# Optimization experiments

Measured on AMD Instinct MI355X. Metric: run time of the kernel, lower is better.

## Reference

```python
import jax, jax.numpy as jnp
import numpy as np

EPS = 1e-5
SCALE_MIN, SCALE_MAX = 0.6, 1.0


def _layer_norm(x):
    m = jnp.mean(x, axis=-1, keepdims=True)
    v = jnp.mean((x - m) ** 2, axis=-1, keepdims=True)
    return (x - m) / jnp.sqrt(v + EPS)


def _scan_dir(seq, A, Bp, Cp, D, W_in, W_out, snr_scale):
    """seq: [B, L, C] -> [B, L, C]. Diagonal SSM recurrence h = A*h + B*u."""
    Bsz, L, C = seq.shape
    N = A.shape[0]
    seq = _layer_norm(seq)
    u = jnp.einsum('blc,nc->bln', seq, W_in)                 # input_proj, [B,L,N]
    A_base = jnp.tanh(A)[None, :]                            # [1,N]
    s = jnp.clip(snr_scale, 0.0, 1.0)[:, None]               # [B,1]
    scale = SCALE_MIN + (SCALE_MAX - SCALE_MIN) * s
    Ad = jnp.clip(A_base * scale, -0.99, 0.99)               # [B,N]
    Bu = Bp[None, None, :] * u                               # [B,L,N]

    def step(h, bu_t):
        h = Ad * h + bu_t
        return h, h

    h0 = jnp.zeros((Bsz, N), dtype=seq.dtype)
    _, hs = jax.lax.scan(step, h0, jnp.swapaxes(Bu, 0, 1))   # hs: [L,B,N]
    hs = jnp.swapaxes(hs, 0, 1)                              # [B,L,N]
    y_state = Cp[None, None, :] * hs
    y = jnp.einsum('bln,cn->blc', y_state, W_out)            # output_proj
    return y + D[None, None, :] * seq


def _forward(x, snr_scale, A, Bparam, Cparam, D, W_in, W_out):
    Bsz, H, W, C = x.shape
    L = H * W
    if L > 4000:
        x = _layer_norm(x)
    # row scans
    seq_row = x.reshape(Bsz, L, C)
    y_row_f = _scan_dir(seq_row, A, Bparam, Cparam, D, W_in, W_out, snr_scale)
    y_row_b = _scan_dir(seq_row[:, ::-1, :], A, Bparam, Cparam, D, W_in, W_out, snr_scale)
    y_row = 0.5 * (y_row_f + y_row_b[:, ::-1, :])
    y_row = y_row.reshape(Bsz, H, W, C)
    # column scans
    x_col = jnp.transpose(x, (0, 2, 1, 3))                   # [B,W,H,C]
    seq_col = x_col.reshape(Bsz, L, C)
    y_col_f = _scan_dir(seq_col, A, Bparam, Cparam, D, W_in, W_out, snr_scale)
    y_col_b = _scan_dir(seq_col[:, ::-1, :], A, Bparam, Cparam, D, W_in, W_out, snr_scale)
    y_col = 0.5 * (y_col_f + y_col_b[:, ::-1, :])
    y_col = jnp.transpose(y_col.reshape(Bsz, W, H, C), (0, 2, 1, 3))
    return 0.5 * (y_row + y_col)


def setup_inputs() -> dict:
    key = jax.random.key(0)
    k = jax.random.split(key, 4)
    Bsz, H, W, C, N = 8, 64, 64, 256, 64
    x = jax.random.normal(k[0], (Bsz, H, W, C), dtype=jnp.float32)
    snr_scale = jax.random.uniform(k[1], (Bsz,), dtype=jnp.float32)
    A = -0.5 * jnp.ones((N,), dtype=jnp.float32)
    Bparam = 0.5 * jnp.ones((N,), dtype=jnp.float32)
    Cparam = 0.5 * jnp.ones((N,), dtype=jnp.float32)
    D = jnp.zeros((C,), dtype=jnp.float32)
    # nn.Linear default init: U(-1/sqrt(fan_in), 1/sqrt(fan_in))
    W_in = jax.random.uniform(k[2], (N, C), dtype=jnp.float32,
                              minval=-1.0 / np.sqrt(C), maxval=1.0 / np.sqrt(C))
    W_out = jax.random.uniform(k[3], (C, N), dtype=jnp.float32,
                               minval=-1.0 / np.sqrt(N), maxval=1.0 / np.sqrt(N))
    return {"x": x, "snr_scale": snr_scale, "A": A, "Bparam": Bparam,
            "Cparam": Cparam, "D": D, "W_in": W_in, "W_out": W_out}


def reference(x, snr_scale, A, Bparam, Cparam, D, W_in, W_out):
    return _forward(x, snr_scale, A, Bparam, Cparam, D, W_in, W_out)
```

## Files before the change

### kernel.cpp

```cpp
#include <hip/hip_runtime.h>
#include <hip/hip_bf16.h>
#include <math.h>

#define Bsz 8
#define Hh 64
#define Ww 64
#define Cc 256
#define Nn 64
#define Ll 4096
#define EPSf 1e-5f

typedef __bf16 v8bf __attribute__((ext_vector_type(8)));
typedef float  f32x4 __attribute__((ext_vector_type(4)));

__device__ __forceinline__ float ad_val(float a, float snr) {
    float s = fminf(fmaxf(snr, 0.f), 1.f);
    float scale = 0.6f + 0.4f * s;
    float v = tanhf(a) * scale;
    return fminf(fmaxf(v, -0.99f), 0.99f);
}

__global__ __launch_bounds__(256) void k0_weights(
    const float* __restrict__ Win, const float* __restrict__ Wout,
    const float* __restrict__ Bp, const float* __restrict__ Cp,
    __bf16* __restrict__ Wh, __bf16* __restrict__ Wl,
    __bf16* __restrict__ Woh, __bf16* __restrict__ Wol,
    float* __restrict__ WB)
{
    const int t = threadIdx.x;
    const int blk = blockIdx.x;
    if (blk < 4) {
        for (int idx = blk * 512 + t; idx < blk * 512 + 512; idx += 256) {
            int tile = idx >> 6, lane = idx & 63;
            int kt = tile >> 2, nt = tile & 3;
            int q = lane >> 4, n = nt * 16 + (lane & 15);
            #pragma unroll
            for (int j = 0; j < 8; ++j) {
                int k = kt * 32 + q * 8 + j;
                float w = Win[n * Cc + k];
                __bf16 h = (__bf16)w;
                Wh[idx * 8 + j] = h;
                Wl[idx * 8 + j] = (__bf16)(w - (float)h);
            }
        }
    } else if (blk < 8) {
        for (int idx = (blk - 4) * 512 + t; idx < (blk - 4) * 512 + 512; idx += 256) {
            int tile = idx >> 6, lane = idx & 63;
            int kt = tile >> 4, ntg = tile & 15;
            int q = lane >> 4, c = ntg * 16 + (lane & 15);
            #pragma unroll
            for (int j = 0; j < 8; ++j) {
                int k = kt * 32 + q * 8 + j;
                float w = Wout[c * Nn + k] * 0.25f * Cp[k];
                __bf16 h = (__bf16)w;
                Woh[idx * 8 + j] = h;
                Wol[idx * 8 + j] = (__bf16)(w - (float)h);
            }
        }
    } else {
        __shared__ float wtmp[256];
        int n = t >> 2, qd = t & 3;
        float s = 0.f;
        const float* wr = Win + (long)n * Cc + qd * 64;
        for (int i = 0; i < 64; ++i) s += wr[i];
        wtmp[t] = s;
        __syncthreads();
        if (t < 64)
            WB[t] = (wtmp[t*4] + wtmp[t*4+1] + wtmp[t*4+2] + wtmp[t*4+3]) * Bp[t];
    }
}

__global__ __launch_bounds__(256) void k1_ln_gemm(
    const float* __restrict__ x, const __bf16* __restrict__ Wh,
    const __bf16* __restrict__ Wl, const float* __restrict__ Bp,
    const float* __restrict__ WB, float* __restrict__ Bu,
    float* __restrict__ Mst, float* __restrict__ Sst)
{
    __shared__ float mrow[64], srow[64];
    const int t = threadIdx.x;
    const int lane = t & 63;
    const int wv = __builtin_amdgcn_readfirstlane(t >> 6);
    const long pbase = (long)blockIdx.x * 64;
    const float* xt = x + pbase * Cc;

    for (int rr = 0; rr < 16; ++rr) {
        int r = wv * 16 + rr;
        float4 v = ((const float4*)(xt + (long)r * Cc))[lane];
        float s = v.x + v.y + v.z + v.w;
        float q = v.x*v.x + v.y*v.y + v.z*v.z + v.w*v.w;
        #pragma unroll
        for (int off = 32; off > 0; off >>= 1) {
            s += __shfl_down(s, off);
            q += __shfl_down(q, off);
        }
        if (lane == 0) {
            float m = s * (1.f/256.f);
            float var = fmaxf(q * (1.f/256.f) - m*m, 0.f);
            float r1 = rsqrtf(var + EPSf);
            float v2 = var / (var + EPSf);
            float sc = r1 * rsqrtf(v2 + EPSf);
            mrow[r] = m; srow[r] = sc;
            Mst[pbase + r] = m; Sst[pbase + r] = sc;
        }
    }
    __syncthreads();

    const int q = lane >> 4;
    const int mi = lane & 15;
    const float* xa = xt + (long)(wv * 16 + mi) * Cc + q * 8;

    f32x4 acc[4];
    #pragma unroll
    for (int nt = 0; nt < 4; ++nt) acc[nt] = (f32x4){0.f, 0.f, 0.f, 0.f};

    #pragma unroll
    for (int kt = 0; kt < 8; ++kt) {
        float4 a0 = *(const float4*)(xa + kt * 32);
        float4 a1 = *(const float4*)(xa + kt * 32 + 4);
        float av[8] = {a0.x, a0.y, a0.z, a0.w, a1.x, a1.y, a1.z, a1.w};
        v8bf ah, al;
        #pragma unroll
        for (int j = 0; j < 8; ++j) {
            __bf16 h = (__bf16)av[j];
            ah[j] = h;
            al[j] = (__bf16)(av[j] - (float)h);
        }
        #pragma unroll
        for (int nt = 0; nt < 4; ++nt) {
            v8bf bh = *(const v8bf*)(Wh + ((long)(kt * 4 + nt) * 64 + lane) * 8);
            v8bf bl = *(const v8bf*)(Wl + ((long)(kt * 4 + nt) * 64 + lane) * 8);
            acc[nt] = __builtin_amdgcn_mfma_f32_16x16x32_bf16(ah, bh, acc[nt], 0, 0, 0);
            acc[nt] = __builtin_amdgcn_mfma_f32_16x16x32_bf16(al, bh, acc[nt], 0, 0, 0);
            acc[nt] = __builtin_amdgcn_mfma_f32_16x16x32_bf16(ah, bl, acc[nt], 0, 0, 0);
        }
    }

    #pragma unroll
    for (int nt = 0; nt < 4; ++nt) {
        int n = nt * 16 + mi;
        float bpn = Bp[n];
        float wbn = WB[n];
        #pragma unroll
        for (int reg = 0; reg < 4; ++reg) {
            int p = wv * 16 + q * 4 + reg;
            float m = mrow[p], s = srow[p];
            Bu[(pbase + p) * Nn + n] = s * (acc[nt][reg] * bpn - m * wbn);
        }
    }
}

__global__ __launch_bounds__(256) void k2_carry(
    const float* __restrict__ Bu, const float* __restrict__ A,
    const float* __restrict__ snr, float* __restrict__ E)
{
    const int t = threadIdx.x;
    const int lane = t & 63;
    const int task = blockIdx.x * 4 + (t >> 6);
    const int isCol = task >> 9;
    const int b = (task >> 6) & 7;
    const int j = task & 63;
    const float Ad = ad_val(A[lane], snr[b]);
    const float* src = Bu + ((long)b * Ll + (isCol ? j : j * 64)) * Nn + lane;
    const long stride = isCol ? (long)Ww * Nn : Nn;

    float v[64];
    #pragma unroll
    for (int k = 0; k < 64; ++k) v[k] = src[k * stride];

    float s = 0.f;
    #pragma unroll
    for (int k = 0; k < 64; ++k) s = fmaf(Ad, s, v[k]);
    const int dF = isCol ? 2 : 0;
    E[((dF * 8 + b) * 64 + j) * 64 + lane] = s;

    float sb = 0.f;
    #pragma unroll
    for (int k = 63; k >= 0; --k) sb = fmaf(Ad, sb, v[k]);
    E[(((dF + 1) * 8 + b) * 64 + (63 - j)) * 64 + lane] = sb;
}

__global__ __launch_bounds__(64) void k3_prefix(
    const float* __restrict__ E, float* __restrict__ CT,
    const float* __restrict__ A, const float* __restrict__ snr)
{
    const int lane = threadIdx.x;
    const int db = blockIdx.x;
    const int b = db & 7;
    float Ad = ad_val(A[lane], snr[b]);
    float p64 = Ad;
    #pragma unroll
    for (int i = 0; i < 6; ++i) p64 *= p64;
    const float* e = E + (long)db * 4096 + lane;
    float* ct = CT + (long)db * 4096 + lane;
    float v[64];
    #pragma unroll
    for (int k = 0; k < 64; ++k) v[k] = e[k * 64];
    float c = 0.f;
    #pragma unroll
    for (int k = 0; k < 64; ++k) {
        ct[k * 64] = c;
        c = fmaf(p64, c, v[k]);
    }
}

__global__ __launch_bounds__(256) void k4_apply(
    const float* __restrict__ Bu, const float* __restrict__ CT,
    const float* __restrict__ A, const float* __restrict__ snr,
    float* __restrict__ Srow, float* __restrict__ Scol)
{
    const int t = threadIdx.x;
    const int lane = t & 63;
    const int task = blockIdx.x * 4 + (t >> 6);
    const int isCol = task >> 9;
    const int b = (task >> 6) & 7;
    const int j = task & 63;
    const float Ad = ad_val(A[lane], snr[b]);
    const float* src = Bu + ((long)b * Ll + (isCol ? j : j * 64)) * Nn + lane;
    const long stride = isCol ? (long)Ww * Nn : Nn;
    const int dF = isCol ? 2 : 0;
    const float cf = CT[((dF * 8 + b) * 64 + j) * 64 + lane];
    const float cb = CT[(((dF + 1) * 8 + b) * 64 + (63 - j)) * 64 + lane];

    float v[64];
    #pragma unroll
    for (int k = 0; k < 64; ++k) v[k] = src[k * stride];

    float hf[64];
    float h = cf;
    #pragma unroll
    for (int k = 0; k < 64; ++k) { h = fmaf(Ad, h, v[k]); hf[k] = h; }

    float* out0 = (isCol ? Scol : Srow) +
                  ((long)b * Ll + (isCol ? j : j * 64)) * Nn + lane;
    float sb = cb;
    #pragma unroll
    for (int k = 63; k >= 0; --k) {
        sb = fmaf(Ad, sb, v[k]);
        out0[k * stride] = hf[k] + sb;
    }
}

__global__ __launch_bounds__(256) void k5_gemm_out(
    const float* __restrict__ Srow, const float* __restrict__ Scol,
    const float* __restrict__ x, const __bf16* __restrict__ Woh,
    const __bf16* __restrict__ Wol, const float* __restrict__ Dp,
    const float* __restrict__ Mst, const float* __restrict__ Sst,
    float* __restrict__ out)
{
    __shared__ float smem[64 * 260];
    const int t = threadIdx.x;
    const int lane = t & 63;
    const int wv = __builtin_amdgcn_readfirstlane(t >> 6);
    const long pbase = (long)blockIdx.x * 64;
    const int q = lane >> 4;
    const int mi = lane & 15;

    const float4* Sr = (const float4*)(Srow + pbase * Nn);
    const float4* Sc = (const float4*)(Scol + pbase * Nn);
    #pragma unroll
    for (int i = 0; i < 4; ++i) {
        int fi = i * 256 + t;
        float4 a = Sr[fi], c = Sc[fi];
        *(float4*)&smem[(fi >> 4) * 68 + (fi & 15) * 4] =
            make_float4(a.x + c.x, a.y + c.y, a.z + c.z, a.w + c.w);
    }
    __syncthreads();

    f32x4 acc[4][4];
    #pragma unroll
    for (int mt = 0; mt < 4; ++mt)
        #pragma unroll
        for (int nt = 0; nt < 4; ++nt) acc[mt][nt] = (f32x4){0.f, 0.f, 0.f, 0.f};

    #pragma unroll
    for (int kt = 0; kt < 2; ++kt) {
        v8bf bh[4], bl[4];
        #pragma unroll
        for (int nt = 0; nt < 4; ++nt) {
            long wo = ((long)(kt * 16 + wv * 4 + nt) * 64 + lane) * 8;
            bh[nt] = *(const v8bf*)(Woh + wo);
            bl[nt] = *(const v8bf*)(Wol + wo);
        }
        #pragma unroll
        for (int mt = 0; mt < 4; ++mt) {
            const float* ar = &smem[(mt * 16 + mi) * 68 + q * 8 + kt * 32];
            v8bf sh, sl;
            #pragma unroll
            for (int j = 0; j < 8; ++j) {
                float sv = ar[j];
                __bf16 hh = (__bf16)sv;
                sh[j] = hh;
                sl[j] = (__bf16)(sv - (float)hh);
            }
            #pragma unroll
            for (int nt = 0; nt < 4; ++nt) {
                acc[mt][nt] = __builtin_amdgcn_mfma_f32_16x16x32_bf16(sh, bh[nt], acc[mt][nt], 0, 0, 0);
                acc[mt][nt] = __builtin_amdgcn_mfma_f32_16x16x32_bf16(sl, bh[nt], acc[mt][nt], 0, 0, 0);
                acc[mt][nt] = __builtin_amdgcn_mfma_f32_16x16x32_bf16(sh, bl[nt], acc[mt][nt], 0, 0, 0);
            }
        }
    }
    __syncthreads();
    #pragma unroll
    for (int mt = 0; mt < 4; ++mt)
        #pragma unroll
        for (int nt = 0; nt < 4; ++nt) {
            int c = wv * 64 + nt * 16 + mi;
            #pragma unroll
            for (int reg = 0; reg < 4; ++reg)
                smem[(mt * 16 + q * 4 + reg) * 260 + c] = acc[mt][nt][reg];
        }
    __syncthreads();

    const float4* xg = (const float4*)(x + pbase * Cc);
    float4* og = (float4*)(out + pbase * Cc);
    const float4 dv = ((const float4*)Dp)[lane];
    #pragma unroll 4
    for (int i = 0; i < 16; ++i) {
        int fi = i * 256 + t;
        int p = i * 4 + wv;
        float4 v = *(const float4*)&smem[p * 260 + lane * 4];
        float m = Mst[pbase + p], s = Sst[pbase + p];
        float4 xv = xg[fi];
        og[fi] = make_float4(v.x + dv.x * ((xv.x - m) * s),
                             v.y + dv.y * ((xv.y - m) * s),
                             v.z + dv.z * ((xv.z - m) * s),
                             v.w + dv.w * ((xv.w - m) * s));
    }
}

extern "C" void kernel_launch(void* const* d_in, const int* in_sizes, int n_in,
                              void* d_out, int out_size, void* d_ws, size_t ws_size,
                              hipStream_t stream)
{
    const float* x    = (const float*)d_in[0];
    const float* snr  = (const float*)d_in[1];
    const float* A    = (const float*)d_in[2];
    const float* Bp   = (const float*)d_in[3];
    const float* Cp   = (const float*)d_in[4];
    const float* Dp   = (const float*)d_in[5];
    const float* Win  = (const float*)d_in[6];
    const float* Wout = (const float*)d_in[7];
    float* out = (float*)d_out;

    char* ws = (char*)d_ws;
    float*  Bu   = (float*)(ws);
    float*  Srow = (float*)(ws + (size_t)8  * 1024 * 1024);
    float*  Scol = (float*)(ws + (size_t)16 * 1024 * 1024);
    float*  E    = (float*)(ws + (size_t)24 * 1024 * 1024);
    float*  CT   = (float*)(ws + (size_t)24 * 1024 * 1024 + 512*1024);
    float*  Mst  = (float*)(ws + (size_t)25 * 1024 * 1024);
    float*  Sst  = (float*)(ws + (size_t)25 * 1024 * 1024 + 128*1024);
    char*   wbase = ws + (size_t)25 * 1024 * 1024 + 512 * 1024;
    __bf16* Wh   = (__bf16*)(wbase);
    __bf16* Wl   = (__bf16*)(wbase + 32 * 1024);
    __bf16* Woh  = (__bf16*)(wbase + 64 * 1024);
    __bf16* Wol  = (__bf16*)(wbase + 96 * 1024);
    float*  WB   = (float*)(wbase + 128 * 1024);

    hipLaunchKernelGGL(k0_weights,  dim3(9),   dim3(256), 0, stream, Win, Wout, Bp, Cp, Wh, Wl, Woh, Wol, WB);
    hipLaunchKernelGGL(k1_ln_gemm,  dim3(512), dim3(256), 0, stream, x, Wh, Wl, Bp, WB, Bu, Mst, Sst);
    hipLaunchKernelGGL(k2_carry,    dim3(256), dim3(256), 0, stream, Bu, A, snr, E);
    hipLaunchKernelGGL(k3_prefix,   dim3(32),  dim3(64),  0, stream, E, CT, A, snr);
    hipLaunchKernelGGL(k4_apply,    dim3(256), dim3(256), 0, stream, Bu, CT, A, snr, Srow, Scol);
    hipLaunchKernelGGL(k5_gemm_out, dim3(512), dim3(256), 0, stream, Srow, Scol, x, Woh, Wol, Dp, Mst, Sst, out);
}
```

Measured before the change: 138.4 us.

## Split scan chunks across wave pairs, fold prefix kernel into apply, halve epilogue LDS

Each 64-step scan chunk is now split across two waves of 32 steps. In the carry kernel the halves are combined through LDS, and partial sums are stored for later seeding. The separate prefix kernel is removed, and the apply kernel recomputes its carry-in by looping serially over the preceding chunk totals. The output GEMM epilogue stages results through LDS in two 32-row halves, halving shared memory to raise occupancy. In exchange, apply threads do redundant serial prefix work of up to 63 strided loads each, and extra syncs are added.

```diff
diff --git a/kernel.cpp b/kernel.cpp
--- a/kernel.cpp
+++ b/kernel.cpp
@@ -151,90 +151,99 @@
 
 __global__ __launch_bounds__(256) void k2_carry(
     const float* __restrict__ Bu, const float* __restrict__ A,
-    const float* __restrict__ snr, float* __restrict__ E)
-{
+    const float* __restrict__ snr, float* __restrict__ E,
+    float* __restrict__ Pf, float* __restrict__ Pb)
+{
+    __shared__ float exch[2][2][64];
     const int t = threadIdx.x;
     const int lane = t & 63;
-    const int task = blockIdx.x * 4 + (t >> 6);
+    const int wv = t >> 6;
+    const int pairIdx = wv >> 1;
+    const int half = wv & 1;
+    const int task = blockIdx.x * 2 + pairIdx;
     const int isCol = task >> 9;
     const int b = (task >> 6) & 7;
     const int j = task & 63;
     const float Ad = ad_val(A[lane], snr[b]);
-    const float* src = Bu + ((long)b * Ll + (isCol ? j : j * 64)) * Nn + lane;
+    float p32 = Ad;
+    #pragma unroll
+    for (int i = 0; i < 5; ++i) p32 *= p32;
     const long stride = isCol ? (long)Ww * Nn : Nn;
-
-    float v[64];
-    #pragma unroll
-    for (int k = 0; k < 64; ++k) v[k] = src[k * stride];
-
-    float s = 0.f;
-    #pragma unroll
-    for (int k = 0; k < 64; ++k) s = fmaf(Ad, s, v[k]);
-    const int dF = isCol ? 2 : 0;
-    E[((dF * 8 + b) * 64 + j) * 64 + lane] = s;
-
-    float sb = 0.f;
-    #pragma unroll
-    for (int k = 63; k >= 0; --k) sb = fmaf(Ad, sb, v[k]);
-    E[(((dF + 1) * 8 + b) * 64 + (63 - j)) * 64 + lane] = sb;
-}
-
-__global__ __launch_bounds__(64) void k3_prefix(
-    const float* __restrict__ E, float* __restrict__ CT,
-    const float* __restrict__ A, const float* __restrict__ snr)
-{
-    const int lane = threadIdx.x;
-    const int db = blockIdx.x;
-    const int b = db & 7;
-    float Ad = ad_val(A[lane], snr[b]);
-    float p64 = Ad;
-    #pragma unroll
-    for (int i = 0; i < 6; ++i) p64 *= p64;
-    const float* e = E + (long)db * 4096 + lane;
-    float* ct = CT + (long)db * 4096 + lane;
-    float v[64];
-    #pragma unroll
-    for (int k = 0; k < 64; ++k) v[k] = e[k * 64];
-    float c = 0.f;
-    #pragma unroll
-    for (int k = 0; k < 64; ++k) {
-        ct[k * 64] = c;
-        c = fmaf(p64, c, v[k]);
+    const float* src = Bu + ((long)b * Ll + (isCol ? j : j * 64)) * Nn
+                       + (long)half * 32 * stride + lane;
+    float v[32];
+    #pragma unroll
+    for (int k = 0; k < 32; ++k) v[k] = src[k * stride];
+    float pf = 0.f;
+    #pragma unroll
+    for (int k = 0; k < 32; ++k) pf = fmaf(Ad, pf, v[k]);
+    float pb = 0.f;
+    #pragma unroll
+    for (int k = 31; k >= 0; --k) pb = fmaf(Ad, pb, v[k]);
+    if (half) { exch[pairIdx][0][lane] = pf; exch[pairIdx][1][lane] = pb; }
+    __syncthreads();
+    if (!half) {
+        const int dF = isCol ? 2 : 0;
+        float pf_hi = exch[pairIdx][0][lane];
+        float pb_hi = exch[pairIdx][1][lane];
+        E[((dF * 8 + b) * 64 + j) * 64 + lane]              = fmaf(p32, pf, pf_hi);
+        E[(((dF + 1) * 8 + b) * 64 + (63 - j)) * 64 + lane] = fmaf(p32, pb_hi, pb);
+        Pf[task * 64 + lane] = pf;
+        Pb[task * 64 + lane] = pb_hi;
     }
 }
 
 __global__ __launch_bounds__(256) void k4_apply(
-    const float* __restrict__ Bu, const float* __restrict__ CT,
+    const float* __restrict__ Bu, const float* __restrict__ E,
+    const float* __restrict__ Pf, const float* __restrict__ Pb,
     const float* __restrict__ A, const float* __restrict__ snr,
     float* __restrict__ Srow, float* __restrict__ Scol)
 {
     const int t = threadIdx.x;
     const int lane = t & 63;
-    const int task = blockIdx.x * 4 + (t >> 6);
+    const int wv = t >> 6;
+    const int task = blockIdx.x * 2 + (wv >> 1);
+    const int half = wv & 1;
     const int isCol = task >> 9;
     const int b = (task >> 6) & 7;
     const int j = task & 63;
     const float Ad = ad_val(A[lane], snr[b]);
-    const float* src = Bu + ((long)b * Ll + (isCol ? j : j * 64)) * Nn + lane;
+    float p32 = Ad;
+    #pragma unroll
+    for (int i = 0; i < 5; ++i) p32 *= p32;
+    float p64 = p32 * p32;
+    const int dF = isCol ? 2 : 0;
+
+    const float* Ef = E + (long)((dF * 8 + b) * 64) * 64 + lane;
+    const float* Eb = E + (long)(((dF + 1) * 8 + b) * 64) * 64 + lane;
+    float cf = 0.f;
+    #pragma unroll 4
+    for (int i = 0; i < j; ++i) cf = fmaf(p64, cf, Ef[i * 64]);
+    float cb = 0.f;
+    const int jj = 63 - j;
+    #pragma unroll 4
+    for (int i = 0; i < jj; ++i) cb = fmaf(p64, cb, Eb[i * 64]);
+
+    float fseed = half ? fmaf(p32, cf, Pf[task * 64 + lane]) : cf;
+    float bseed = half ? cb : fmaf(p32, cb, Pb[task * 64 + lane]);
+
     const long stride = isCol ? (long)Ww * Nn : Nn;
-    const int dF = isCol ? 2 : 0;
-    const float cf = CT[((dF * 8 + b) * 64 + j) * 64 + lane];
-    const float cb = CT[(((dF + 1) * 8 + b) * 64 + (63 - j)) * 64 + lane];
-
-    float v[64];
-    #pragma unroll
-    for (int k = 0; k < 64; ++k) v[k] = src[k * stride];
-
-    float hf[64];
-    float h = cf;
-    #pragma unroll
-    for (int k = 0; k < 64; ++k) { h = fmaf(Ad, h, v[k]); hf[k] = h; }
-
-    float* out0 = (isCol ? Scol : Srow) +
-                  ((long)b * Ll + (isCol ? j : j * 64)) * Nn + lane;
-    float sb = cb;
-    #pragma unroll
-    for (int k = 63; k >= 0; --k) {
+    const long base = ((long)b * Ll + (isCol ? j : j * 64)) * Nn
+                      + (long)half * 32 * stride + lane;
+    const float* src = Bu + base;
+    float v[32];
+    #pragma unroll
+    for (int k = 0; k < 32; ++k) v[k] = src[k * stride];
+
+    float hf[32];
+    float h = fseed;
+    #pragma unroll
+    for (int k = 0; k < 32; ++k) { h = fmaf(Ad, h, v[k]); hf[k] = h; }
+
+    float* out0 = (isCol ? Scol : Srow) + base;
+    float sb = bseed;
+    #pragma unroll
+    for (int k = 31; k >= 0; --k) {
         sb = fmaf(Ad, sb, v[k]);
         out0[k * stride] = hf[k] + sb;
     }
@@ -247,7 +256,7 @@
     const float* __restrict__ Mst, const float* __restrict__ Sst,
     float* __restrict__ out)
 {
-    __shared__ float smem[64 * 260];
+    __shared__ float smem[32 * 260];
     const int t = threadIdx.x;
     const int lane = t & 63;
     const int wv = __builtin_amdgcn_readfirstlane(t >> 6);
@@ -300,32 +309,39 @@
             }
         }
     }
-    __syncthreads();
-    #pragma unroll
-    for (int mt = 0; mt < 4; ++mt)
-        #pragma unroll
-        for (int nt = 0; nt < 4; ++nt) {
-            int c = wv * 64 + nt * 16 + mi;
-            #pragma unroll
-            for (int reg = 0; reg < 4; ++reg)
-                smem[(mt * 16 + q * 4 + reg) * 260 + c] = acc[mt][nt][reg];
-        }
-    __syncthreads();
 
     const float4* xg = (const float4*)(x + pbase * Cc);
     float4* og = (float4*)(out + pbase * Cc);
     const float4 dv = ((const float4*)Dp)[lane];
-    #pragma unroll 4
-    for (int i = 0; i < 16; ++i) {
-        int fi = i * 256 + t;
-        int p = i * 4 + wv;
-        float4 v = *(const float4*)&smem[p * 260 + lane * 4];
-        float m = Mst[pbase + p], s = Sst[pbase + p];
-        float4 xv = xg[fi];
-        og[fi] = make_float4(v.x + dv.x * ((xv.x - m) * s),
-                             v.y + dv.y * ((xv.y - m) * s),
-                             v.z + dv.z * ((xv.z - m) * s),
-                             v.w + dv.w * ((xv.w - m) * s));
+    #pragma unroll
+    for (int hh = 0; hh < 2; ++hh) {
+        __syncthreads();
+        #pragma unroll
+        for (int mt2 = 0; mt2 < 2; ++mt2) {
+            int mt = hh * 2 + mt2;
+            #pragma unroll
+            for (int nt = 0; nt < 4; ++nt) {
+                int c = wv * 64 + nt * 16 + mi;
+                #pragma unroll
+                for (int reg = 0; reg < 4; ++reg)
+                    smem[(mt2 * 16 + q * 4 + reg) * 260 + c] = acc[mt][nt][reg];
+            }
+        }
+        __syncthreads();
+        #pragma unroll 4
+        for (int i = 0; i < 8; ++i) {
+            int fi = i * 256 + t;
+            int pl = i * 4 + wv;
+            long pg = pbase + hh * 32 + pl;
+            float4 vv = *(const float4*)&smem[pl * 260 + lane * 4];
+            float m = Mst[pg], s = Sst[pg];
+            float4 xv = xg[hh * 2048 + fi];
+            og[hh * 2048 + fi] = make_float4(
+                vv.x + dv.x * ((xv.x - m) * s),
+                vv.y + dv.y * ((xv.y - m) * s),
+                vv.z + dv.z * ((xv.z - m) * s),
+                vv.w + dv.w * ((xv.w - m) * s));
+        }
     }
 }
 
@@ -348,7 +364,8 @@
     float*  Srow = (float*)(ws + (size_t)8  * 1024 * 1024);
     float*  Scol = (float*)(ws + (size_t)16 * 1024 * 1024);
     float*  E    = (float*)(ws + (size_t)24 * 1024 * 1024);
-    float*  CT   = (float*)(ws + (size_t)24 * 1024 * 1024 + 512*1024);
+    float*  Pf   = (float*)(ws + (size_t)24 * 1024 * 1024 + 512*1024);
+    float*  Pb   = (float*)(ws + (size_t)24 * 1024 * 1024 + 768*1024);
     float*  Mst  = (float*)(ws + (size_t)25 * 1024 * 1024);
     float*  Sst  = (float*)(ws + (size_t)25 * 1024 * 1024 + 128*1024);
     char*   wbase = ws + (size_t)25 * 1024 * 1024 + 512 * 1024;
@@ -360,8 +377,7 @@
 
     hipLaunchKernelGGL(k0_weights,  dim3(9),   dim3(256), 0, stream, Win, Wout, Bp, Cp, Wh, Wl, Woh, Wol, WB);
     hipLaunchKernelGGL(k1_ln_gemm,  dim3(512), dim3(256), 0, stream, x, Wh, Wl, Bp, WB, Bu, Mst, Sst);
-    hipLaunchKernelGGL(k2_carry,    dim3(256), dim3(256), 0, stream, Bu, A, snr, E);
-    hipLaunchKernelGGL(k3_prefix,   dim3(32),  dim3(64),  0, stream, E, CT, A, snr);
-    hipLaunchKernelGGL(k4_apply,    dim3(256), dim3(256), 0, stream, Bu, CT, A, snr, Srow, Scol);
+    hipLaunchKernelGGL(k2_carry,    dim3(512), dim3(256), 0, stream, Bu, A, snr, E, Pf, Pb);
+    hipLaunchKernelGGL(k4_apply,    dim3(512), dim3(256), 0, stream, Bu, E, Pf, Pb, A, snr, Srow, Scol);
     hipLaunchKernelGGL(k5_gemm_out, dim3(512), dim3(256), 0, stream, Srow, Scol, x, Woh, Wol, Dp, Mst, Sst, out);
 }
```

New measurement: 156.1 us. +12.8%, slower.

## Fuse row-direction scan carry and apply into the input and output GEMM kernels

Applied to the files above, without the earlier changes.

The row-direction scan work moves out of the standalone carry and apply kernels. k1 now computes each block's row-segment carries from the Bu tile it has just produced in shared memory. k5 recomputes the row-direction scan states locally from Bu and the prefix carries, then adds the column states before the output GEMM. This removes the Srow buffer and its global write and read, and halves the grid of the column-only scan kernels. In exchange, k5 uses more shared memory and more barriers, and its epilogue staging is split into two halves to fit the smaller buffer.

```diff
diff --git a/kernel.cpp b/kernel.cpp
--- a/kernel.cpp
+++ b/kernel.cpp
@@ -73,29 +73,34 @@
 __global__ __launch_bounds__(256) void k1_ln_gemm(
     const float* __restrict__ x, const __bf16* __restrict__ Wh,
     const __bf16* __restrict__ Wl, const float* __restrict__ Bp,
-    const float* __restrict__ WB, float* __restrict__ Bu,
-    float* __restrict__ Mst, float* __restrict__ Sst)
-{
+    const float* __restrict__ WB, const float* __restrict__ A,
+    const float* __restrict__ snr, float* __restrict__ Bu,
+    float* __restrict__ E, float* __restrict__ Mst, float* __restrict__ Sst)
+{
+    __shared__ float zs[64 * 68];
+    __shared__ float exch[8 * 64];
     __shared__ float mrow[64], srow[64];
     const int t = threadIdx.x;
     const int lane = t & 63;
     const int wv = __builtin_amdgcn_readfirstlane(t >> 6);
     const long pbase = (long)blockIdx.x * 64;
+    const int b = blockIdx.x >> 6;
+    const int j = blockIdx.x & 63;
     const float* xt = x + pbase * Cc;
 
     for (int rr = 0; rr < 16; ++rr) {
         int r = wv * 16 + rr;
         float4 v = ((const float4*)(xt + (long)r * Cc))[lane];
         float s = v.x + v.y + v.z + v.w;
-        float q = v.x*v.x + v.y*v.y + v.z*v.z + v.w*v.w;
+        float qq = v.x*v.x + v.y*v.y + v.z*v.z + v.w*v.w;
         #pragma unroll
         for (int off = 32; off > 0; off >>= 1) {
             s += __shfl_down(s, off);
-            q += __shfl_down(q, off);
+            qq += __shfl_down(qq, off);
         }
         if (lane == 0) {
             float m = s * (1.f/256.f);
-            float var = fmaxf(q * (1.f/256.f) - m*m, 0.f);
+            float var = fmaxf(qq * (1.f/256.f) - m*m, 0.f);
             float r1 = rsqrtf(var + EPSf);
             float v2 = var / (var + EPSf);
             float sc = r1 * rsqrtf(v2 + EPSf);
@@ -120,10 +125,10 @@
         float av[8] = {a0.x, a0.y, a0.z, a0.w, a1.x, a1.y, a1.z, a1.w};
         v8bf ah, al;
         #pragma unroll
-        for (int j = 0; j < 8; ++j) {
-            __bf16 h = (__bf16)av[j];
-            ah[j] = h;
-            al[j] = (__bf16)(av[j] - (float)h);
+        for (int jj = 0; jj < 8; ++jj) {
+            __bf16 h = (__bf16)av[jj];
+            ah[jj] = h;
+            al[jj] = (__bf16)(av[jj] - (float)h);
         }
         #pragma unroll
         for (int nt = 0; nt < 4; ++nt) {
@@ -144,24 +149,57 @@
         for (int reg = 0; reg < 4; ++reg) {
             int p = wv * 16 + q * 4 + reg;
             float m = mrow[p], s = srow[p];
-            Bu[(pbase + p) * Nn + n] = s * (acc[nt][reg] * bpn - m * wbn);
-        }
-    }
-}
-
-__global__ __launch_bounds__(256) void k2_carry(
+            zs[p * 68 + n] = s * (acc[nt][reg] * bpn - m * wbn);
+        }
+    }
+    __syncthreads();
+    float4* bug = (float4*)(Bu + pbase * Nn);
+    #pragma unroll
+    for (int i = 0; i < 4; ++i) {
+        int fi = i * 256 + t;
+        bug[fi] = *(const float4*)&zs[(fi >> 4) * 68 + (fi & 15) * 4];
+    }
+    const float Ad = ad_val(A[lane], snr[b]);
+    float v[16];
+    #pragma unroll
+    for (int k = 0; k < 16; ++k) v[k] = zs[(wv * 16 + k) * 68 + lane];
+    float pf = 0.f, pb = 0.f;
+    #pragma unroll
+    for (int k = 0; k < 16; ++k) pf = fmaf(Ad, pf, v[k]);
+    #pragma unroll
+    for (int k = 15; k >= 0; --k) pb = fmaf(Ad, pb, v[k]);
+    exch[wv * 64 + lane] = pf;
+    exch[(4 + wv) * 64 + lane] = pb;
+    __syncthreads();
+    if (t < 64) {
+        float p16 = Ad;
+        #pragma unroll
+        for (int i = 0; i < 4; ++i) p16 *= p16;
+        float ef = exch[lane];
+        ef = fmaf(p16, ef, exch[64 + lane]);
+        ef = fmaf(p16, ef, exch[128 + lane]);
+        ef = fmaf(p16, ef, exch[192 + lane]);
+        E[((0 * 8 + b) * 64 + j) * 64 + lane] = ef;
+        float eb = exch[(4 + 3) * 64 + lane];
+        eb = fmaf(p16, eb, exch[(4 + 2) * 64 + lane]);
+        eb = fmaf(p16, eb, exch[(4 + 1) * 64 + lane]);
+        eb = fmaf(p16, eb, exch[(4 + 0) * 64 + lane]);
+        E[((1 * 8 + b) * 64 + (63 - j)) * 64 + lane] = eb;
+    }
+}
+
+__global__ __launch_bounds__(256) void k2_col(
     const float* __restrict__ Bu, const float* __restrict__ A,
     const float* __restrict__ snr, float* __restrict__ E)
 {
     const int t = threadIdx.x;
     const int lane = t & 63;
     const int task = blockIdx.x * 4 + (t >> 6);
-    const int isCol = task >> 9;
     const int b = (task >> 6) & 7;
     const int j = task & 63;
     const float Ad = ad_val(A[lane], snr[b]);
-    const float* src = Bu + ((long)b * Ll + (isCol ? j : j * 64)) * Nn + lane;
-    const long stride = isCol ? (long)Ww * Nn : Nn;
+    const float* src = Bu + ((long)b * Ll + j) * Nn + lane;
+    const long stride = (long)Ww * Nn;
 
     float v[64];
     #pragma unroll
@@ -170,13 +208,12 @@
     float s = 0.f;
     #pragma unroll
     for (int k = 0; k < 64; ++k) s = fmaf(Ad, s, v[k]);
-    const int dF = isCol ? 2 : 0;
-    E[((dF * 8 + b) * 64 + j) * 64 + lane] = s;
+    E[((2 * 8 + b) * 64 + j) * 64 + lane] = s;
 
     float sb = 0.f;
     #pragma unroll
     for (int k = 63; k >= 0; --k) sb = fmaf(Ad, sb, v[k]);
-    E[(((dF + 1) * 8 + b) * 64 + (63 - j)) * 64 + lane] = sb;
+    E[((3 * 8 + b) * 64 + (63 - j)) * 64 + lane] = sb;
 }
 
 __global__ __launch_bounds__(64) void k3_prefix(
@@ -203,23 +240,21 @@
     }
 }
 
-__global__ __launch_bounds__(256) void k4_apply(
+__global__ __launch_bounds__(256) void k4_col(
     const float* __restrict__ Bu, const float* __restrict__ CT,
     const float* __restrict__ A, const float* __restrict__ snr,
-    float* __restrict__ Srow, float* __restrict__ Scol)
+    float* __restrict__ Scol)
 {
     const int t = threadIdx.x;
     const int lane = t & 63;
     const int task = blockIdx.x * 4 + (t >> 6);
-    const int isCol = task >> 9;
     const int b = (task >> 6) & 7;
     const int j = task & 63;
     const float Ad = ad_val(A[lane], snr[b]);
-    const float* src = Bu + ((long)b * Ll + (isCol ? j : j * 64)) * Nn + lane;
-    const long stride = isCol ? (long)Ww * Nn : Nn;
-    const int dF = isCol ? 2 : 0;
-    const float cf = CT[((dF * 8 + b) * 64 + j) * 64 + lane];
-    const float cb = CT[(((dF + 1) * 8 + b) * 64 + (63 - j)) * 64 + lane];
+    const float* src = Bu + ((long)b * Ll + j) * Nn + lane;
+    const long stride = (long)Ww * Nn;
+    const float cf = CT[((2 * 8 + b) * 64 + j) * 64 + lane];
+    const float cb = CT[((3 * 8 + b) * 64 + (63 - j)) * 64 + lane];
 
     float v[64];
     #pragma unroll
@@ -230,8 +265,7 @@
     #pragma unroll
     for (int k = 0; k < 64; ++k) { h = fmaf(Ad, h, v[k]); hf[k] = h; }
 
-    float* out0 = (isCol ? Scol : Srow) +
-                  ((long)b * Ll + (isCol ? j : j * 64)) * Nn + lane;
+    float* out0 = Scol + ((long)b * Ll + j) * Nn + lane;
     float sb = cb;
     #pragma unroll
     for (int k = 63; k >= 0; --k) {
@@ -240,29 +274,75 @@
     }
 }
 
-__global__ __launch_bounds__(256) void k5_gemm_out(
-    const float* __restrict__ Srow, const float* __restrict__ Scol,
-    const float* __restrict__ x, const __bf16* __restrict__ Woh,
-    const __bf16* __restrict__ Wol, const float* __restrict__ Dp,
-    const float* __restrict__ Mst, const float* __restrict__ Sst,
-    float* __restrict__ out)
-{
-    __shared__ float smem[64 * 260];
+__global__ __launch_bounds__(256) void k5_fused(
+    const float* __restrict__ Bu, const float* __restrict__ Scol,
+    const float* __restrict__ CT, const float* __restrict__ x,
+    const __bf16* __restrict__ Woh, const __bf16* __restrict__ Wol,
+    const float* __restrict__ A, const float* __restrict__ snr,
+    const float* __restrict__ Dp, const float* __restrict__ Mst,
+    const float* __restrict__ Sst, float* __restrict__ out)
+{
+    __shared__ float smem[8320];
+    __shared__ float exch[8 * 64];
     const int t = threadIdx.x;
     const int lane = t & 63;
     const int wv = __builtin_amdgcn_readfirstlane(t >> 6);
+    const int b = blockIdx.x >> 6;
+    const int j = blockIdx.x & 63;
     const long pbase = (long)blockIdx.x * 64;
     const int q = lane >> 4;
     const int mi = lane & 15;
 
-    const float4* Sr = (const float4*)(Srow + pbase * Nn);
-    const float4* Sc = (const float4*)(Scol + pbase * Nn);
+    const float4* Bg = (const float4*)(Bu + pbase * Nn);
     #pragma unroll
     for (int i = 0; i < 4; ++i) {
         int fi = i * 256 + t;
-        float4 a = Sr[fi], c = Sc[fi];
-        *(float4*)&smem[(fi >> 4) * 68 + (fi & 15) * 4] =
-            make_float4(a.x + c.x, a.y + c.y, a.z + c.z, a.w + c.w);
+        *(float4*)&smem[(fi >> 4) * 68 + (fi & 15) * 4] = Bg[fi];
+    }
+    __syncthreads();
+
+    const float Ad = ad_val(A[lane], snr[b]);
+    float p16 = Ad;
+    #pragma unroll
+    for (int i = 0; i < 4; ++i) p16 *= p16;
+    float v[16];
+    #pragma unroll
+    for (int k = 0; k < 16; ++k) v[k] = smem[(wv * 16 + k) * 68 + lane];
+    float pf = 0.f, pb = 0.f;
+    #pragma unroll
+    for (int k = 0; k < 16; ++k) pf = fmaf(Ad, pf, v[k]);
+    #pragma unroll
+    for (int k = 15; k >= 0; --k) pb = fmaf(Ad, pb, v[k]);
+    exch[wv * 64 + lane] = pf;
+    exch[(4 + wv) * 64 + lane] = pb;
+    const float cf = CT[((0 * 8 + b) * 64 + j) * 64 + lane];
+    const float cb = CT[((1 * 8 + b) * 64 + (63 - j)) * 64 + lane];
+    __syncthreads();
+    float cw = cf;
+    for (int wq = 0; wq < wv; ++wq) cw = fmaf(p16, cw, exch[wq * 64 + lane]);
+    float dw = cb;
+    for (int wq = 3; wq > wv; --wq) dw = fmaf(p16, dw, exch[(4 + wq) * 64 + lane]);
+
+    float hf[16];
+    float h = cw;
+    #pragma unroll
+    for (int k = 0; k < 16; ++k) { h = fmaf(Ad, h, v[k]); hf[k] = h; }
+    float sb = dw;
+    #pragma unroll
+    for (int k = 15; k >= 0; --k) {
+        sb = fmaf(Ad, sb, v[k]);
+        smem[(wv * 16 + k) * 68 + lane] = hf[k] + sb;
+    }
+    __syncthreads();
+
+    const float4* Sc = (const float4*)(Scol + pbase * Nn);
+    #pragma unroll
+    for (int i = 0; i < 4; ++i) {
+        int fi = i * 256 + t;
+        float* d = &smem[(fi >> 4) * 68 + (fi & 15) * 4];
+        float4 c = Sc[fi];
+        float4 cur = *(const float4*)d;
+        *(float4*)d = make_float4(cur.x + c.x, cur.y + c.y, cur.z + c.z, cur.w + c.w);
     }
     __syncthreads();
 
@@ -286,11 +366,11 @@
             const float* ar = &smem[(mt * 16 + mi) * 68 + q * 8 + kt * 32];
             v8bf sh, sl;
             #pragma unroll
-            for (int j = 0; j < 8; ++j) {
-                float sv = ar[j];
+            for (int jj = 0; jj < 8; ++jj) {
+                float sv = ar[jj];
                 __bf16 hh = (__bf16)sv;
-                sh[j] = hh;
-                sl[j] = (__bf16)(sv - (float)hh);
+                sh[jj] = hh;
+                sl[jj] = (__bf16)(sv - (float)hh);
             }
             #pragma unroll
             for (int nt = 0; nt < 4; ++nt) {
@@ -300,32 +380,39 @@
             }
         }
     }
-    __syncthreads();
-    #pragma unroll
-    for (int mt = 0; mt < 4; ++mt)
-        #pragma unroll
-        for (int nt = 0; nt < 4; ++nt) {
-            int c = wv * 64 + nt * 16 + mi;
-            #pragma unroll
-            for (int reg = 0; reg < 4; ++reg)
-                smem[(mt * 16 + q * 4 + reg) * 260 + c] = acc[mt][nt][reg];
-        }
-    __syncthreads();
 
     const float4* xg = (const float4*)(x + pbase * Cc);
     float4* og = (float4*)(out + pbase * Cc);
     const float4 dv = ((const float4*)Dp)[lane];
-    #pragma unroll 4
-    for (int i = 0; i < 16; ++i) {
-        int fi = i * 256 + t;
-        int p = i * 4 + wv;
-        float4 v = *(const float4*)&smem[p * 260 + lane * 4];
-        float m = Mst[pbase + p], s = Sst[pbase + p];
-        float4 xv = xg[fi];
-        og[fi] = make_float4(v.x + dv.x * ((xv.x - m) * s),
-                             v.y + dv.y * ((xv.y - m) * s),
-                             v.z + dv.z * ((xv.z - m) * s),
-                             v.w + dv.w * ((xv.w - m) * s));
+    #pragma unroll
+    for (int hh = 0; hh < 2; ++hh) {
+        __syncthreads();
+        #pragma unroll
+        for (int mt2 = 0; mt2 < 2; ++mt2) {
+            int mt = hh * 2 + mt2;
+            #pragma unroll
+            for (int nt = 0; nt < 4; ++nt) {
+                int c = wv * 64 + nt * 16 + mi;
+                #pragma unroll
+                for (int reg = 0; reg < 4; ++reg)
+                    smem[(mt2 * 16 + q * 4 + reg) * 260 + c] = acc[mt][nt][reg];
+            }
+        }
+        __syncthreads();
+        #pragma unroll 4
+        for (int i = 0; i < 8; ++i) {
+            int fi = i * 256 + t;
+            int pl = i * 4 + wv;
+            long pg = pbase + hh * 32 + pl;
+            float4 vv = *(const float4*)&smem[pl * 260 + lane * 4];
+            float m = Mst[pg], s = Sst[pg];
+            float4 xv = xg[hh * 2048 + fi];
+            og[hh * 2048 + fi] = make_float4(
+                vv.x + dv.x * ((xv.x - m) * s),
+                vv.y + dv.y * ((xv.y - m) * s),
+                vv.z + dv.z * ((xv.z - m) * s),
+                vv.w + dv.w * ((xv.w - m) * s));
+        }
     }
 }
 
@@ -345,23 +432,22 @@
 
     char* ws = (char*)d_ws;
     float*  Bu   = (float*)(ws);
-    float*  Srow = (float*)(ws + (size_t)8  * 1024 * 1024);
-    float*  Scol = (float*)(ws + (size_t)16 * 1024 * 1024);
-    float*  E    = (float*)(ws + (size_t)24 * 1024 * 1024);
-    float*  CT   = (float*)(ws + (size_t)24 * 1024 * 1024 + 512*1024);
-    float*  Mst  = (float*)(ws + (size_t)25 * 1024 * 1024);
-    float*  Sst  = (float*)(ws + (size_t)25 * 1024 * 1024 + 128*1024);
-    char*   wbase = ws + (size_t)25 * 1024 * 1024 + 512 * 1024;
+    float*  Scol = (float*)(ws + (size_t)8  * 1024 * 1024);
+    float*  E    = (float*)(ws + (size_t)16 * 1024 * 1024);
+    float*  CT   = (float*)(ws + (size_t)16 * 1024 * 1024 + 512*1024);
+    float*  Mst  = (float*)(ws + (size_t)17 * 1024 * 1024);
+    float*  Sst  = (float*)(ws + (size_t)17 * 1024 * 1024 + 128*1024);
+    char*   wbase = ws + (size_t)18 * 1024 * 1024;
     __bf16* Wh   = (__bf16*)(wbase);
     __bf16* Wl   = (__bf16*)(wbase + 32 * 1024);
     __bf16* Woh  = (__bf16*)(wbase + 64 * 1024);
     __bf16* Wol  = (__bf16*)(wbase + 96 * 1024);
     float*  WB   = (float*)(wbase + 128 * 1024);
 
-    hipLaunchKernelGGL(k0_weights,  dim3(9),   dim3(256), 0, stream, Win, Wout, Bp, Cp, Wh, Wl, Woh, Wol, WB);
-    hipLaunchKernelGGL(k1_ln_gemm,  dim3(512), dim3(256), 0, stream, x, Wh, Wl, Bp, WB, Bu, Mst, Sst);
-    hipLaunchKernelGGL(k2_carry,    dim3(256), dim3(256), 0, stream, Bu, A, snr, E);
-    hipLaunchKernelGGL(k3_prefix,   dim3(32),  dim3(64),  0, stream, E, CT, A, snr);
-    hipLaunchKernelGGL(k4_apply,    dim3(256), dim3(256), 0, stream, Bu, CT, A, snr, Srow, Scol);
-    hipLaunchKernelGGL(k5_gemm_out, dim3(512), dim3(256), 0, stream, Srow, Scol, x, Woh, Wol, Dp, Mst, Sst, out);
-}
+    hipLaunchKernelGGL(k0_weights, dim3(9),   dim3(256), 0, stream, Win, Wout, Bp, Cp, Wh, Wl, Woh, Wol, WB);
+    hipLaunchKernelGGL(k1_ln_gemm, dim3(512), dim3(256), 0, stream, x, Wh, Wl, Bp, WB, A, snr, Bu, E, Mst, Sst);
+    hipLaunchKernelGGL(k2_col,     dim3(128), dim3(256), 0, stream, Bu, A, snr, E);
+    hipLaunchKernelGGL(k3_prefix,  dim3(32),  dim3(64),  0, stream, E, CT, A, snr);
+    hipLaunchKernelGGL(k4_col,     dim3(128), dim3(256), 0, stream, Bu, CT, A, snr, Scol);
+    hipLaunchKernelGGL(k5_fused,   dim3(512), dim3(256), 0, stream, Bu, Scol, CT, x, Woh, Wol, A, snr, Dp, Mst, Sst, out);
+}
```

Result: slower. 142.5 us (+2.9%).
